# Optimization experiments

Hardware: AMD Instinct MI355X
Metric: run time of the kernel (lower is better)

The kernel has to match this reference:

```python
import jax, jax.numpy as jnp
import numpy as np

B, T, IN, CTRL = 128, 64, 512, 512
N, MM, S, R, W = 128, 128, 3, 4, 1  # slots, word size, num_shift, read heads, write heads
L = 3 + MM + S          # per-read-head instr length (k,b,g,s,t)
LW = L + 2 * MM         # per-write-head instr length (+erase,+add)
NOUT = R * L + W * LW   # 926


def _l2n(x, axis):
    # matches tf.nn.l2_normalize: x * rsqrt(max(sum(x^2), 1e-12))
    return x * jax.lax.rsqrt(jnp.maximum(jnp.sum(x * x, axis=axis, keepdims=True), 1e-12))


def _get_weight(Mem, w_old, head):
    # Mem (B,N,MM), w_old (B,N), head (B,L)
    k = head[:, :MM]
    b = jnp.exp(head[:, MM])
    g = jax.nn.sigmoid(head[:, MM + 1])
    s = jax.nn.softmax(head[:, MM + 2:MM + 2 + S], axis=-1)
    t = jax.nn.softplus(head[:, MM + 2 + S]) + 1.0
    # content addressing (NB: original normalizes M along axis=1, the slot axis -- kept faithful)
    nM = _l2n(Mem, 1)
    nk = _l2n(k, -1)
    sim = jnp.einsum('bnm,bm->bn', nM, nk)
    wc = jax.nn.softmax(sim * b[:, None], axis=-1)
    # interpolate
    wi = wc * g[:, None] + w_old * (1.0 - g[:, None])
    # circular shift via small correlation window
    bound = S // 2
    padded = jnp.concatenate([wi[:, -bound:], wi, wi[:, :bound]], axis=1)  # (B, N+2*bound)
    win = jnp.stack([padded[:, j:j + N] for j in range(S)], axis=-1)       # (B,N,S)
    ws = jnp.einsum('bns,bs->bn', win, s)
    # sharpen
    p = jnp.power(ws, t[:, None])
    return p / (jnp.sum(p, axis=-1, keepdims=True) + 1e-12)


def _forward(x, Wc, bc, Wk, bk):
    Mem0 = jnp.zeros((B, N, MM), x.dtype).at[:, N // 2, :].set(1.0)
    rv0 = jnp.zeros((B, R, MM), x.dtype)
    rw0 = jnp.zeros((B, R, N), x.dtype)
    ww0 = jnp.zeros((B, W, N), x.dtype)
    gw = jax.vmap(_get_weight, in_axes=(None, 1, 1), out_axes=1)  # over head axis

    def step(carry, xt):
        rv, rw, ww, Mem = carry
        h = jnp.concatenate([xt, rv.reshape(B, R * MM)], axis=-1)
        out = jnp.tanh(h @ Wc + bc)               # controller output
        instrs = out @ Wk + bk                    # head instructions (B,NOUT)
        rh = instrs[:, :R * L].reshape(B, R, L)
        wh = instrs[:, R * L:].reshape(B, W, LW)
        rw_new = gw(Mem, rw, rh)                  # (B,R,N)
        ww_new = gw(Mem, ww, wh[..., :L])         # (B,W,N)
        e = wh[..., L:L + MM]                     # (B,W,MM)
        a = wh[..., L + MM:]                      # (B,W,MM)
        for i in range(W):                        # erase all heads first
            Mem = Mem * (1.0 - ww_new[:, i, :, None] * e[:, i, None, :])
        for i in range(W):                        # then add
            Mem = Mem + ww_new[:, i, :, None] * a[:, i, None, :]
        rv_new = jnp.einsum('bnm,brn->brm', Mem, rw_new)
        return (rv_new, rw_new, ww_new, Mem), out

    _, outs = jax.lax.scan(step, (rv0, rw0, ww0, Mem0), jnp.swapaxes(x, 0, 1))
    return jnp.swapaxes(outs, 0, 1)  # (B,T,CTRL) return_sequences=True


def setup_inputs() -> dict:
    key = jax.random.key(0)
    ks = jax.random.split(key, 3)
    x = jax.random.normal(ks[0], (B, T, IN), jnp.float32)
    Wc = jax.random.normal(ks[1], (IN + R * MM, CTRL), jnp.float32) / np.sqrt(IN + R * MM).astype(np.float32)
    bc = jnp.zeros((CTRL,), jnp.float32)
    Wk = jax.random.normal(ks[2], (CTRL, NOUT), jnp.float32) * 0.02
    bk = jnp.zeros((NOUT,), jnp.float32)
    return {"x": x, "Wc": Wc, "bc": bc, "Wk": Wk, "bk": bk}


def reference(x, Wc, bc, Wk, bk):
    return _forward(x, Wc, bc, Wk, bk)
```

## Files before the change

### kernel.cpp

```cpp
#include <hip/hip_runtime.h>
#include <math.h>

#define B_    128
#define T_    64
#define INX   512
#define CTRL  512
#define NN    128
#define MMM   128
#define RR    4
#define LLh   134
#define NOUT  926
#define NTHR  512

#define MSTR  129

struct __align__(16) SM2 {
  float Mem[2][NN][MSTR];
  float rw[2][RR][NN];
  float ww[2][NN];
  float instr[2][928];
  float rv[2][512];
  union {
    float out_s[2][512];
    struct { float red[2][256]; float invn[2][MMM]; } d;
  } u;
};

__device__ __forceinline__ float wsum64(float v) {
  #pragma unroll
  for (int m = 32; m >= 1; m >>= 1) v += __shfl_xor(v, m);
  return v;
}
__device__ __forceinline__ float wmax64(float v) {
  #pragma unroll
  for (int m = 32; m >= 1; m >>= 1) v = fmaxf(v, __shfl_xor(v, m));
  return v;
}

__global__ __launch_bounds__(256) void pre_mm(const float* __restrict__ X,
                                              const float* __restrict__ Wc,
                                              const float* __restrict__ bc,
                                              float* __restrict__ out) {
  __shared__ float Xs[16][68];
  __shared__ float Ws[16][64];
  const int wg = blockIdx.x;
  const int r0 = (wg >> 3) * 64, c0 = (wg & 7) * 64;
  const int tid = threadIdx.x;
  const int ti = tid >> 4, tj = tid & 15;
  float acc[4][4] = {};
  for (int kk = 0; kk < 512; kk += 16) {
    __syncthreads();
    for (int e = tid; e < 1024; e += 256) {
      int i = e >> 4, k = e & 15;
      Xs[k][i] = X[(size_t)(r0 + i) * 512 + kk + k];
    }
    for (int e = tid; e < 1024; e += 256) {
      int k = e >> 6, j = e & 63;
      Ws[k][j] = Wc[(size_t)(kk + k) * CTRL + c0 + j];
    }
    __syncthreads();
    #pragma unroll
    for (int k = 0; k < 16; ++k) {
      float a0 = Xs[k][ti*4+0], a1 = Xs[k][ti*4+1], a2 = Xs[k][ti*4+2], a3 = Xs[k][ti*4+3];
      float b0 = Ws[k][tj*4+0], b1 = Ws[k][tj*4+1], b2 = Ws[k][tj*4+2], b3 = Ws[k][tj*4+3];
      acc[0][0]+=a0*b0; acc[0][1]+=a0*b1; acc[0][2]+=a0*b2; acc[0][3]+=a0*b3;
      acc[1][0]+=a1*b0; acc[1][1]+=a1*b1; acc[1][2]+=a1*b2; acc[1][3]+=a1*b3;
      acc[2][0]+=a2*b0; acc[2][1]+=a2*b1; acc[2][2]+=a2*b2; acc[2][3]+=a2*b3;
      acc[3][0]+=a3*b0; acc[3][1]+=a3*b1; acc[3][2]+=a3*b2; acc[3][3]+=a3*b3;
    }
  }
  #pragma unroll
  for (int i = 0; i < 4; ++i) {
    size_t o = (size_t)(r0 + ti*4 + i) * 512 + c0 + tj*4;
    float4 v = { acc[i][0] + bc[c0+tj*4+0], acc[i][1] + bc[c0+tj*4+1],
                 acc[i][2] + bc[c0+tj*4+2], acc[i][3] + bc[c0+tj*4+3] };
    *(float4*)&out[o] = v;
  }
}

__device__ __forceinline__ void do_head(SM2& sm, int tau, int lane) {
  const int b  = tau / 5;
  const int hd = tau - 5 * b;
  const int off = (hd < RR) ? hd * LLh : RR * LLh;
  const float* ins = sm.instr[b];
  const int n0 = lane, n1 = lane + 64;

  float k0 = ins[off + n0], k1 = ins[off + n1];
  float invk = rsqrtf(fmaxf(wsum64(k0 * k0 + k1 * k1), 1e-12f));
  float beta = expf(ins[off + 128]);
  float gg = 1.f / (1.f + expf(-ins[off + 129]));
  float s0 = ins[off + 130], s1 = ins[off + 131], s2 = ins[off + 132];
  float smx = fmaxf(s0, fmaxf(s1, s2));
  float e0 = expf(s0 - smx), e1 = expf(s1 - smx), e2 = expf(s2 - smx);
  float esm = e0 + e1 + e2; s0 = e0 / esm; s1 = e1 / esm; s2 = e2 / esm;
  float spx = ins[off + 133];
  float tt = ((spx > 20.f) ? spx : log1pf(expf(spx))) + 1.0f;

  float p0 = 0.f, p1 = 0.f;
  #pragma unroll 4
  for (int m = 0; m < 128; ++m) {
    float km = sm.u.d.invn[b][m] * ins[off + m];
    p0 += sm.Mem[b][n0][m] * km;
    p1 += sm.Mem[b][n1][m] * km;
  }
  float sim0 = p0 * invk * beta, sim1 = p1 * invk * beta;
  float mx = wmax64(fmaxf(sim0, sim1));
  float ev0 = expf(sim0 - mx), ev1 = expf(sim1 - mx);
  float es = wsum64(ev0 + ev1);
  float wold0 = (hd < RR) ? sm.rw[b][hd][n0] : sm.ww[b][n0];
  float wold1 = (hd < RR) ? sm.rw[b][hd][n1] : sm.ww[b][n1];
  float wi0 = gg * (ev0 / es) + (1.f - gg) * wold0;
  float wi1 = gg * (ev1 / es) + (1.f - gg) * wold1;

  int ls = (lane + 63) & 63;
  float A0 = __shfl(wi0, ls), A1 = __shfl(wi1, ls);
  float wprev0 = (lane == 0) ? A1 : A0;
  float wprev1 = (lane == 0) ? A0 : A1;
  int ln = (lane + 1) & 63;
  float B0 = __shfl(wi0, ln), B1 = __shfl(wi1, ln);
  float wnext0 = (lane == 63) ? B1 : B0;
  float wnext1 = (lane == 63) ? B0 : B1;

  float ws0 = s0 * wprev0 + s1 * wi0 + s2 * wnext0;
  float ws1 = s0 * wprev1 + s1 * wi1 + s2 * wnext1;
  float pv0 = powf(ws0, tt), pv1 = powf(ws1, tt);
  float inv = 1.f / (wsum64(pv0 + pv1) + 1e-12f);
  if (hd < RR) { sm.rw[b][hd][n0] = pv0 * inv; sm.rw[b][hd][n1] = pv1 * inv; }
  else         { sm.ww[b][n0]     = pv0 * inv; sm.ww[b][n1]     = pv1 * inv; }
}

__global__ __launch_bounds__(512) void ntm2(const float* __restrict__ Wc,
                                            const float* __restrict__ Wk,
                                            const float* __restrict__ bk,
                                            float* __restrict__ out) {
  __shared__ SM2 sm;
  const int wg = blockIdx.x, tid = threadIdx.x;
  const int b0 = wg * 2;
  const int lt = tid & 255, bb = tid >> 8;
  const int j  = tid;
  const int wv = tid >> 6, lane = tid & 63;

  for (int e = tid; e < 2 * NN * MMM; e += NTHR) {
    int bl = e >> 14, n = (e >> 7) & 127;
    sm.Mem[bl][n][e & 127] = (n == NN / 2) ? 1.0f : 0.0f;
  }
  for (int e = tid; e < 2 * RR * NN; e += NTHR) ((float*)sm.rw)[e] = 0.0f;
  for (int e = tid; e < 2 * NN;      e += NTHR) ((float*)sm.ww)[e] = 0.0f;
  for (int e = tid; e < 2 * 512;     e += NTHR) ((float*)sm.rv)[e] = 0.0f;
  __syncthreads();

  for (int t = 0; t < T_; ++t) {
    {
      float a0 = 0.f, a1 = 0.f;
      const float* wp = Wc + (size_t)INX * CTRL + j;
      for (int k8 = 0; k8 < 512; k8 += 8) {
        float w0 = wp[(size_t)(k8+0)*CTRL];
        float w1 = wp[(size_t)(k8+1)*CTRL];
        float w2 = wp[(size_t)(k8+2)*CTRL];
        float w3 = wp[(size_t)(k8+3)*CTRL];
        float w4 = wp[(size_t)(k8+4)*CTRL];
        float w5 = wp[(size_t)(k8+5)*CTRL];
        float w6 = wp[(size_t)(k8+6)*CTRL];
        float w7 = wp[(size_t)(k8+7)*CTRL];
        float4 r0a = *(const float4*)&sm.rv[0][k8];
        float4 r0b = *(const float4*)&sm.rv[0][k8+4];
        float4 r1a = *(const float4*)&sm.rv[1][k8];
        float4 r1b = *(const float4*)&sm.rv[1][k8+4];
        a0 += r0a.x*w0 + r0a.y*w1 + r0a.z*w2 + r0a.w*w3
            + r0b.x*w4 + r0b.y*w5 + r0b.z*w6 + r0b.w*w7;
        a1 += r1a.x*w0 + r1a.y*w1 + r1a.z*w2 + r1a.w*w3
            + r1b.x*w4 + r1b.y*w5 + r1b.z*w6 + r1b.w*w7;
      }
      size_t o0 = ((size_t)(b0+0)*T_ + t)*CTRL + j;
      size_t o1 = ((size_t)(b0+1)*T_ + t)*CTRL + j;
      float v0 = tanhf(out[o0] + a0);
      float v1 = tanhf(out[o1] + a1);
      out[o0] = v0; out[o1] = v1;
      sm.u.out_s[0][j] = v0; sm.u.out_s[1][j] = v1;
    }
    __syncthreads();

    {
      const int c1 = (j < NOUT - 512) ? j + 512 : j;
      float a00 = 0.f, a10 = 0.f, a01 = 0.f, a11 = 0.f;
      const float* wp0 = Wk + j;
      const float* wp1 = Wk + c1;
      for (int k4 = 0; k4 < 512; k4 += 4) {
        float4 o0 = *(const float4*)&sm.u.out_s[0][k4];
        float4 o1 = *(const float4*)&sm.u.out_s[1][k4];
        #pragma unroll
        for (int i = 0; i < 4; ++i) {
          float w0 = wp0[(size_t)(k4+i)*NOUT];
          float w1 = wp1[(size_t)(k4+i)*NOUT];
          float e0 = (i==0)? o0.x : (i==1)? o0.y : (i==2)? o0.z : o0.w;
          float e1 = (i==0)? o1.x : (i==1)? o1.y : (i==2)? o1.z : o1.w;
          a00 += e0 * w0; a01 += e0 * w1;
          a10 += e1 * w0; a11 += e1 * w1;
        }
      }
      sm.instr[0][j] = a00 + bk[j];
      sm.instr[1][j] = a10 + bk[j];
      if (j < NOUT - 512) {
        sm.instr[0][j+512] = a01 + bk[j+512];
        sm.instr[1][j+512] = a11 + bk[j+512];
      }
    }
    __syncthreads();

    {
      {
        int m = lt & 127, h = lt >> 7;
        float p = 0.f;
        #pragma unroll 8
        for (int q = 0; q < 64; ++q) { float v = sm.Mem[bb][h*64+q][m]; p += v*v; }
        sm.u.d.red[bb][lt] = p;
      }
      __syncthreads();
      if (lt < 128) sm.u.d.invn[bb][lt] =
          rsqrtf(fmaxf(sm.u.d.red[bb][lt] + sm.u.d.red[bb][lt+128], 1e-12f));
      __syncthreads();

      do_head(sm, wv, lane);
      if (wv < 2) do_head(sm, 8 + wv, lane);
      __syncthreads();

      for (int e = lt; e < NN * MMM; e += 256) {
        int n = e >> 7, m = e & 127;
        float w = sm.ww[bb][n];
        sm.Mem[bb][n][m] = sm.Mem[bb][n][m] * (1.f - w * sm.instr[bb][670 + m])
                         + w * sm.instr[bb][798 + m];
      }
      __syncthreads();

      for (int e = lt; e < RR * MMM; e += 256) {
        int r = e >> 7, m = e & 127;
        float acc = 0.f;
        #pragma unroll 8
        for (int n = 0; n < NN; ++n) acc += sm.Mem[bb][n][m] * sm.rw[bb][r][n];
        sm.rv[bb][e] = acc;
      }
    }
    __syncthreads();
  }
}

extern "C" void kernel_launch(void* const* d_in, const int* in_sizes, int n_in,
                              void* d_out, int out_size, void* d_ws, size_t ws_size,
                              hipStream_t stream) {
  const float* x  = (const float*)d_in[0];
  const float* Wc = (const float*)d_in[1];
  const float* bc = (const float*)d_in[2];
  const float* Wk = (const float*)d_in[3];
  const float* bk = (const float*)d_in[4];
  float* out = (float*)d_out;

  pre_mm<<<dim3(1024), dim3(256), 0, stream>>>(x, Wc, bc, out);
  ntm2<<<dim3(B_ / 2), dim3(NTHR), 0, stream>>>(Wc, Wk, bk, out);
}
```

Before: 3.188 ms.

## Double recurrent block to 1024 threads with split-K matvecs

Raises the per-block thread count from 512 to 1024. Both recurrent matvecs (rv@Wc and out@Wk) are split along K into two halves, with a shared-memory reduction and an extra barrier each. The slot-norm, head evaluation, memory update and read loops are redistributed over twice as many threads, so each thread does less serial work on the latency-bound per-step chain. The cost is extra barriers and shared traffic per step, and possibly more register pressure under the 1024-thread bound.

```diff
diff --git a/kernel.cpp b/kernel.cpp
--- a/kernel.cpp
+++ b/kernel.cpp
@@ -10,7 +10,7 @@
 #define RR    4
 #define LLh   134
 #define NOUT  926
-#define NTHR  512
+#define NTHR  1024
 
 #define MSTR  129
 
@@ -21,8 +21,8 @@
   float instr[2][928];
   float rv[2][512];
   union {
-    float out_s[2][512];
-    struct { float red[2][256]; float invn[2][MMM]; } d;
+    struct { float out_s[2][512]; float red[512][4]; } c;
+    struct { float red[2][512]; float invn[2][MMM]; } d;
   } u;
 };
 
@@ -55,8 +55,8 @@
       Xs[k][i] = X[(size_t)(r0 + i) * 512 + kk + k];
     }
     for (int e = tid; e < 1024; e += 256) {
-      int k = e >> 6, j = e & 63;
-      Ws[k][j] = Wc[(size_t)(kk + k) * CTRL + c0 + j];
+      int k = e >> 6, jx = e & 63;
+      Ws[k][jx] = Wc[(size_t)(kk + k) * CTRL + c0 + jx];
     }
     __syncthreads();
     #pragma unroll
@@ -129,15 +129,16 @@
   else         { sm.ww[b][n0]     = pv0 * inv; sm.ww[b][n1]     = pv1 * inv; }
 }
 
-__global__ __launch_bounds__(512) void ntm2(const float* __restrict__ Wc,
-                                            const float* __restrict__ Wk,
-                                            const float* __restrict__ bk,
-                                            float* __restrict__ out) {
+__global__ __launch_bounds__(1024) void ntm2(const float* __restrict__ Wc,
+                                             const float* __restrict__ Wk,
+                                             const float* __restrict__ bk,
+                                             float* __restrict__ out) {
   __shared__ SM2 sm;
   const int wg = blockIdx.x, tid = threadIdx.x;
   const int b0 = wg * 2;
-  const int lt = tid & 255, bb = tid >> 8;
-  const int j  = tid;
+  const int j  = tid & 511;
+  const int kh = tid >> 9;
+  const int lt = tid & 511, bb = tid >> 9;
   const int wv = tid >> 6, lane = tid & 63;
 
   for (int e = tid; e < 2 * NN * MMM; e += NTHR) {
@@ -151,9 +152,10 @@
 
   for (int t = 0; t < T_; ++t) {
     {
+      const int kb = kh * 256;
       float a0 = 0.f, a1 = 0.f;
-      const float* wp = Wc + (size_t)INX * CTRL + j;
-      for (int k8 = 0; k8 < 512; k8 += 8) {
+      const float* wp = Wc + (size_t)(INX + kb) * CTRL + j;
+      for (int k8 = 0; k8 < 256; k8 += 8) {
         float w0 = wp[(size_t)(k8+0)*CTRL];
         float w1 = wp[(size_t)(k8+1)*CTRL];
         float w2 = wp[(size_t)(k8+2)*CTRL];
@@ -162,32 +164,39 @@
         float w5 = wp[(size_t)(k8+5)*CTRL];
         float w6 = wp[(size_t)(k8+6)*CTRL];
         float w7 = wp[(size_t)(k8+7)*CTRL];
-        float4 r0a = *(const float4*)&sm.rv[0][k8];
-        float4 r0b = *(const float4*)&sm.rv[0][k8+4];
-        float4 r1a = *(const float4*)&sm.rv[1][k8];
-        float4 r1b = *(const float4*)&sm.rv[1][k8+4];
+        float4 r0a = *(const float4*)&sm.rv[0][kb+k8];
+        float4 r0b = *(const float4*)&sm.rv[0][kb+k8+4];
+        float4 r1a = *(const float4*)&sm.rv[1][kb+k8];
+        float4 r1b = *(const float4*)&sm.rv[1][kb+k8+4];
         a0 += r0a.x*w0 + r0a.y*w1 + r0a.z*w2 + r0a.w*w3
             + r0b.x*w4 + r0b.y*w5 + r0b.z*w6 + r0b.w*w7;
         a1 += r1a.x*w0 + r1a.y*w1 + r1a.z*w2 + r1a.w*w3
             + r1b.x*w4 + r1b.y*w5 + r1b.z*w6 + r1b.w*w7;
       }
-      size_t o0 = ((size_t)(b0+0)*T_ + t)*CTRL + j;
-      size_t o1 = ((size_t)(b0+1)*T_ + t)*CTRL + j;
-      float v0 = tanhf(out[o0] + a0);
-      float v1 = tanhf(out[o1] + a1);
-      out[o0] = v0; out[o1] = v1;
-      sm.u.out_s[0][j] = v0; sm.u.out_s[1][j] = v1;
+      if (kh == 1) { sm.u.c.red[j][0] = a0; sm.u.c.red[j][1] = a1; }
+      __syncthreads();
+      if (kh == 0) {
+        a0 += sm.u.c.red[j][0];
+        a1 += sm.u.c.red[j][1];
+        size_t o0 = ((size_t)(b0+0)*T_ + t)*CTRL + j;
+        size_t o1 = ((size_t)(b0+1)*T_ + t)*CTRL + j;
+        float v0 = tanhf(out[o0] + a0);
+        float v1 = tanhf(out[o1] + a1);
+        out[o0] = v0; out[o1] = v1;
+        sm.u.c.out_s[0][j] = v0; sm.u.c.out_s[1][j] = v1;
+      }
     }
     __syncthreads();
 
     {
+      const int kb = kh * 256;
       const int c1 = (j < NOUT - 512) ? j + 512 : j;
       float a00 = 0.f, a10 = 0.f, a01 = 0.f, a11 = 0.f;
-      const float* wp0 = Wk + j;
-      const float* wp1 = Wk + c1;
-      for (int k4 = 0; k4 < 512; k4 += 4) {
-        float4 o0 = *(const float4*)&sm.u.out_s[0][k4];
-        float4 o1 = *(const float4*)&sm.u.out_s[1][k4];
+      const float* wp0 = Wk + (size_t)kb * NOUT + j;
+      const float* wp1 = Wk + (size_t)kb * NOUT + c1;
+      for (int k4 = 0; k4 < 256; k4 += 4) {
+        float4 o0 = *(const float4*)&sm.u.c.out_s[0][kb + k4];
+        float4 o1 = *(const float4*)&sm.u.c.out_s[1][kb + k4];
         #pragma unroll
         for (int i = 0; i < 4; ++i) {
           float w0 = wp0[(size_t)(k4+i)*NOUT];
@@ -198,11 +207,20 @@
           a10 += e1 * w0; a11 += e1 * w1;
         }
       }
-      sm.instr[0][j] = a00 + bk[j];
-      sm.instr[1][j] = a10 + bk[j];
-      if (j < NOUT - 512) {
-        sm.instr[0][j+512] = a01 + bk[j+512];
-        sm.instr[1][j+512] = a11 + bk[j+512];
+      if (kh == 1) {
+        float4 v = { a00, a01, a10, a11 };
+        *(float4*)&sm.u.c.red[j][0] = v;
+      }
+      __syncthreads();
+      if (kh == 0) {
+        float4 q = *(const float4*)&sm.u.c.red[j][0];
+        a00 += q.x; a01 += q.y; a10 += q.z; a11 += q.w;
+        sm.instr[0][j] = a00 + bk[j];
+        sm.instr[1][j] = a10 + bk[j];
+        if (j < NOUT - 512) {
+          sm.instr[0][j+512] = a01 + bk[j+512];
+          sm.instr[1][j+512] = a11 + bk[j+512];
+        }
       }
     }
     __syncthreads();
@@ -212,32 +230,33 @@
         int m = lt & 127, h = lt >> 7;
         float p = 0.f;
         #pragma unroll 8
-        for (int q = 0; q < 64; ++q) { float v = sm.Mem[bb][h*64+q][m]; p += v*v; }
+        for (int q = 0; q < 32; ++q) { float v = sm.Mem[bb][h*32+q][m]; p += v*v; }
         sm.u.d.red[bb][lt] = p;
       }
       __syncthreads();
       if (lt < 128) sm.u.d.invn[bb][lt] =
-          rsqrtf(fmaxf(sm.u.d.red[bb][lt] + sm.u.d.red[bb][lt+128], 1e-12f));
-      __syncthreads();
-
-      do_head(sm, wv, lane);
-      if (wv < 2) do_head(sm, 8 + wv, lane);
-      __syncthreads();
-
-      for (int e = lt; e < NN * MMM; e += 256) {
-        int n = e >> 7, m = e & 127;
-        float w = sm.ww[bb][n];
-        sm.Mem[bb][n][m] = sm.Mem[bb][n][m] * (1.f - w * sm.instr[bb][670 + m])
-                         + w * sm.instr[bb][798 + m];
-      }
-      __syncthreads();
-
-      for (int e = lt; e < RR * MMM; e += 256) {
-        int r = e >> 7, m = e & 127;
+          rsqrtf(fmaxf(sm.u.d.red[bb][lt] + sm.u.d.red[bb][lt+128]
+                     + sm.u.d.red[bb][lt+256] + sm.u.d.red[bb][lt+384], 1e-12f));
+      __syncthreads();
+
+      if (wv < 10) do_head(sm, wv, lane);
+      __syncthreads();
+
+      for (int e = tid; e < 2 * NN * MMM; e += NTHR) {
+        int bl = e >> 14, n = (e >> 7) & 127, m = e & 127;
+        float w = sm.ww[bl][n];
+        sm.Mem[bl][n][m] = sm.Mem[bl][n][m] * (1.f - w * sm.instr[bl][670 + m])
+                         + w * sm.instr[bl][798 + m];
+      }
+      __syncthreads();
+
+      {
+        int m = tid & 127, r = (tid >> 7) & 3, bl = tid >> 9;
         float acc = 0.f;
+        const float* rwr = sm.rw[bl][r];
         #pragma unroll 8
-        for (int n = 0; n < NN; ++n) acc += sm.Mem[bb][n][m] * sm.rw[bb][r][n];
-        sm.rv[bb][e] = acc;
+        for (int n = 0; n < NN; ++n) acc += sm.Mem[bl][n][m] * rwr[n];
+        sm.rv[bl][r * 128 + m] = acc;
       }
     }
     __syncthreads();
```

After: 2.880 ms. 9.7% less time.

## Split recurrent step across 256 workgroups with global-memory counters between stages

Applied to the files above, without the earlier changes.

Replaces the 64-workgroup kernel, where each workgroup ran the whole time loop for two batch rows, with a 256-workgroup persistent kernel. The controller matmul is tiled over 16-row by 16-column blocks, the instruction matmul over 16-row by 32-column blocks, and the memory and head update runs with one workgroup per batch row. Stages hand off data through global scratch buffers and atomic counters with spin-waits, so the weight reads are spread over more compute units instead of every workgroup streaming all of Wc and Wk. In exchange it adds global round-trips and inter-workgroup synchronization three times per timestep, and it relies on all 256 workgroups being resident at the same time.

```diff
diff --git a/kernel.cpp b/kernel.cpp
--- a/kernel.cpp
+++ b/kernel.cpp
@@ -10,21 +10,33 @@
 #define RR    4
 #define LLh   134
 #define NOUT  926
-#define NTHR  512
-
-#define MSTR  129
-
-struct __align__(16) SM2 {
-  float Mem[2][NN][MSTR];
-  float rw[2][RR][NN];
-  float ww[2][NN];
-  float instr[2][928];
-  float rv[2][512];
-  union {
-    float out_s[2][512];
-    struct { float red[2][256]; float invn[2][MMM]; } d;
-  } u;
+#define NWG   256
+#define NTHR  1024
+
+
+struct __align__(16) SMX {
+  float Mem[NN][129];
+  float rw[RR][NN];
+  float ww[NN];
+  float instr[928];
+  float invn[MMM];
+  float red[1024];
+  float stage[16][512];
 };
+
+__device__ __forceinline__ void spin_ge(int* p, int target) {
+  int it = 0;
+  while (__hip_atomic_load(p, __ATOMIC_RELAXED, __HIP_MEMORY_SCOPE_AGENT) < target) {
+    __builtin_amdgcn_s_sleep(8);
+    if ((++it & 15) == 0) __builtin_amdgcn_fence(__ATOMIC_ACQUIRE, "agent");
+    if (it > (1 << 18)) break;
+  }
+  __builtin_amdgcn_fence(__ATOMIC_ACQUIRE, "agent");
+}
+__device__ __forceinline__ void arrive(int* p) {
+  __builtin_amdgcn_fence(__ATOMIC_RELEASE, "agent");
+  __hip_atomic_fetch_add(p, 1, __ATOMIC_RELAXED, __HIP_MEMORY_SCOPE_AGENT);
+}
 
 __device__ __forceinline__ float wsum64(float v) {
   #pragma unroll
@@ -55,8 +67,8 @@
       Xs[k][i] = X[(size_t)(r0 + i) * 512 + kk + k];
     }
     for (int e = tid; e < 1024; e += 256) {
-      int k = e >> 6, j = e & 63;
-      Ws[k][j] = Wc[(size_t)(kk + k) * CTRL + c0 + j];
+      int k = e >> 6, jx = e & 63;
+      Ws[k][jx] = Wc[(size_t)(kk + k) * CTRL + c0 + jx];
     }
     __syncthreads();
     #pragma unroll
@@ -78,11 +90,9 @@
   }
 }
 
-__device__ __forceinline__ void do_head(SM2& sm, int tau, int lane) {
-  const int b  = tau / 5;
-  const int hd = tau - 5 * b;
+__device__ __forceinline__ void do_head(SMX& sm, int hd, int lane) {
   const int off = (hd < RR) ? hd * LLh : RR * LLh;
-  const float* ins = sm.instr[b];
+  const float* ins = sm.instr;
   const int n0 = lane, n1 = lane + 64;
 
   float k0 = ins[off + n0], k1 = ins[off + n1];
@@ -99,16 +109,16 @@
   float p0 = 0.f, p1 = 0.f;
   #pragma unroll 4
   for (int m = 0; m < 128; ++m) {
-    float km = sm.u.d.invn[b][m] * ins[off + m];
-    p0 += sm.Mem[b][n0][m] * km;
-    p1 += sm.Mem[b][n1][m] * km;
+    float km = sm.invn[m] * ins[off + m];
+    p0 += sm.Mem[n0][m] * km;
+    p1 += sm.Mem[n1][m] * km;
   }
   float sim0 = p0 * invk * beta, sim1 = p1 * invk * beta;
   float mx = wmax64(fmaxf(sim0, sim1));
   float ev0 = expf(sim0 - mx), ev1 = expf(sim1 - mx);
   float es = wsum64(ev0 + ev1);
-  float wold0 = (hd < RR) ? sm.rw[b][hd][n0] : sm.ww[b][n0];
-  float wold1 = (hd < RR) ? sm.rw[b][hd][n1] : sm.ww[b][n1];
+  float wold0 = (hd < RR) ? sm.rw[hd][n0] : sm.ww[n0];
+  float wold1 = (hd < RR) ? sm.rw[hd][n1] : sm.ww[n1];
   float wi0 = gg * (ev0 / es) + (1.f - gg) * wold0;
   float wi1 = gg * (ev1 / es) + (1.f - gg) * wold1;
 
@@ -125,122 +135,150 @@
   float ws1 = s0 * wprev1 + s1 * wi1 + s2 * wnext1;
   float pv0 = powf(ws0, tt), pv1 = powf(ws1, tt);
   float inv = 1.f / (wsum64(pv0 + pv1) + 1e-12f);
-  if (hd < RR) { sm.rw[b][hd][n0] = pv0 * inv; sm.rw[b][hd][n1] = pv1 * inv; }
-  else         { sm.ww[b][n0]     = pv0 * inv; sm.ww[b][n1]     = pv1 * inv; }
-}
-
-__global__ __launch_bounds__(512) void ntm2(const float* __restrict__ Wc,
-                                            const float* __restrict__ Wk,
-                                            const float* __restrict__ bk,
-                                            float* __restrict__ out) {
-  __shared__ SM2 sm;
+  if (hd < RR) { sm.rw[hd][n0] = pv0 * inv; sm.rw[hd][n1] = pv1 * inv; }
+  else         { sm.ww[n0]     = pv0 * inv; sm.ww[n1]     = pv1 * inv; }
+}
+
+__global__ __launch_bounds__(1024) void ntm3(const float* __restrict__ Wc,
+                                             const float* __restrict__ Wk,
+                                             const float* __restrict__ bk,
+                                             float* __restrict__ out,
+                                             float* __restrict__ instr_g,
+                                             float* __restrict__ rv_g,
+                                             int* __restrict__ cnt) {
+  __shared__ SMX sm;
   const int wg = blockIdx.x, tid = threadIdx.x;
-  const int b0 = wg * 2;
-  const int lt = tid & 255, bb = tid >> 8;
-  const int j  = tid;
-  const int wv = tid >> 6, lane = tid & 63;
-
-  for (int e = tid; e < 2 * NN * MMM; e += NTHR) {
-    int bl = e >> 14, n = (e >> 7) & 127;
-    sm.Mem[bl][n][e & 127] = (n == NN / 2) ? 1.0f : 0.0f;
-  }
-  for (int e = tid; e < 2 * RR * NN; e += NTHR) ((float*)sm.rw)[e] = 0.0f;
-  for (int e = tid; e < 2 * NN;      e += NTHR) ((float*)sm.ww)[e] = 0.0f;
-  for (int e = tid; e < 2 * 512;     e += NTHR) ((float*)sm.rv)[e] = 0.0f;
+  const int lane = tid & 63, wv = tid >> 6;
+
+  const int rowgB = wg >> 5, colgB = wg & 31;
+  const int hasC  = (wg < 232);
+  const int rowgC = wg / 29, colgC = wg - rowgC * 29;
+  const int isOwner = (wg < B_);
+  const int bD = wg;
+
+  int* cntB = cnt;
+  int* cntC = cnt + 128;
+  int* cntD = cnt + 256;
+
+  if (isOwner) {
+    for (int e = tid; e < NN * MMM; e += NTHR) {
+      int n = e >> 7;
+      sm.Mem[n][e & 127] = (n == NN / 2) ? 1.0f : 0.0f;
+    }
+    for (int e = tid; e < RR * NN; e += NTHR) ((float*)sm.rw)[e] = 0.0f;
+    if (tid < NN) sm.ww[tid] = 0.0f;
+    if (tid < 512) rv_g[(size_t)bD * 512 + tid] = 0.0f;
+    __syncthreads();
+    if (tid == 0) arrive(&cntD[(bD >> 4) * 16]);
+  }
   __syncthreads();
 
   for (int t = 0; t < T_; ++t) {
+    if (tid == 0) spin_ge(&cntD[rowgB * 16], 16 * (t + 1));
+    __syncthreads();
     {
-      float a0 = 0.f, a1 = 0.f;
-      const float* wp = Wc + (size_t)INX * CTRL + j;
-      for (int k8 = 0; k8 < 512; k8 += 8) {
-        float w0 = wp[(size_t)(k8+0)*CTRL];
-        float w1 = wp[(size_t)(k8+1)*CTRL];
-        float w2 = wp[(size_t)(k8+2)*CTRL];
-        float w3 = wp[(size_t)(k8+3)*CTRL];
-        float w4 = wp[(size_t)(k8+4)*CTRL];
-        float w5 = wp[(size_t)(k8+5)*CTRL];
-        float w6 = wp[(size_t)(k8+6)*CTRL];
-        float w7 = wp[(size_t)(k8+7)*CTRL];
-        float4 r0a = *(const float4*)&sm.rv[0][k8];
-        float4 r0b = *(const float4*)&sm.rv[0][k8+4];
-        float4 r1a = *(const float4*)&sm.rv[1][k8];
-        float4 r1b = *(const float4*)&sm.rv[1][k8+4];
-        a0 += r0a.x*w0 + r0a.y*w1 + r0a.z*w2 + r0a.w*w3
-            + r0b.x*w4 + r0b.y*w5 + r0b.z*w6 + r0b.w*w7;
-        a1 += r1a.x*w0 + r1a.y*w1 + r1a.z*w2 + r1a.w*w3
-            + r1b.x*w4 + r1b.y*w5 + r1b.z*w6 + r1b.w*w7;
-      }
-      size_t o0 = ((size_t)(b0+0)*T_ + t)*CTRL + j;
-      size_t o1 = ((size_t)(b0+1)*T_ + t)*CTRL + j;
-      float v0 = tanhf(out[o0] + a0);
-      float v1 = tanhf(out[o1] + a1);
-      out[o0] = v0; out[o1] = v1;
-      sm.u.out_s[0][j] = v0; sm.u.out_s[1][j] = v1;
-    }
-    __syncthreads();
-
-    {
-      const int c1 = (j < NOUT - 512) ? j + 512 : j;
-      float a00 = 0.f, a10 = 0.f, a01 = 0.f, a11 = 0.f;
-      const float* wp0 = Wk + j;
-      const float* wp1 = Wk + c1;
-      for (int k4 = 0; k4 < 512; k4 += 4) {
-        float4 o0 = *(const float4*)&sm.u.out_s[0][k4];
-        float4 o1 = *(const float4*)&sm.u.out_s[1][k4];
-        #pragma unroll
-        for (int i = 0; i < 4; ++i) {
-          float w0 = wp0[(size_t)(k4+i)*NOUT];
-          float w1 = wp1[(size_t)(k4+i)*NOUT];
-          float e0 = (i==0)? o0.x : (i==1)? o0.y : (i==2)? o0.z : o0.w;
-          float e1 = (i==0)? o1.x : (i==1)? o1.y : (i==2)? o1.z : o1.w;
-          a00 += e0 * w0; a01 += e0 * w1;
-          a10 += e1 * w0; a11 += e1 * w1;
-        }
-      }
-      sm.instr[0][j] = a00 + bk[j];
-      sm.instr[1][j] = a10 + bk[j];
-      if (j < NOUT - 512) {
-        sm.instr[0][j+512] = a01 + bk[j+512];
-        sm.instr[1][j+512] = a11 + bk[j+512];
-      }
-    }
-    __syncthreads();
-
-    {
+      const int b0 = rowgB * 16, c0 = colgB * 16;
+      for (int e = tid * 4; e < 8192; e += NTHR * 4) {
+        int i = e >> 9, k = e & 511;
+        *(float4*)&sm.stage[i][k] = *(const float4*)&rv_g[(size_t)(b0 + i) * 512 + k];
+      }
+      __syncthreads();
+      const int kh = tid >> 8, i = (tid >> 4) & 15, jc = tid & 15;
+      const float* wp = Wc + (size_t)(INX + kh * 128) * CTRL + c0 + jc;
+      const float* rvrow = &sm.stage[i][kh * 128];
+      float a = 0.f;
+      for (int k8 = 0; k8 < 128; k8 += 8) {
+        float w0 = wp[(size_t)(k8+0)*CTRL], w1 = wp[(size_t)(k8+1)*CTRL];
+        float w2 = wp[(size_t)(k8+2)*CTRL], w3 = wp[(size_t)(k8+3)*CTRL];
+        float w4 = wp[(size_t)(k8+4)*CTRL], w5 = wp[(size_t)(k8+5)*CTRL];
+        float w6 = wp[(size_t)(k8+6)*CTRL], w7 = wp[(size_t)(k8+7)*CTRL];
+        a += rvrow[k8+0]*w0 + rvrow[k8+1]*w1 + rvrow[k8+2]*w2 + rvrow[k8+3]*w3
+           + rvrow[k8+4]*w4 + rvrow[k8+5]*w5 + rvrow[k8+6]*w6 + rvrow[k8+7]*w7;
+      }
+      if (kh > 0) sm.red[(kh - 1) * 256 + i * 16 + jc] = a;
+      __syncthreads();
+      if (kh == 0) {
+        a += sm.red[i*16+jc] + sm.red[256 + i*16+jc] + sm.red[512 + i*16+jc];
+        size_t o = ((size_t)(b0 + i) * T_ + t) * CTRL + c0 + jc;
+        out[o] = tanhf(out[o] + a);
+      }
+    }
+    __syncthreads();
+    if (tid == 0) arrive(&cntB[rowgB * 16]);
+
+    if (hasC) {
+      if (tid == 0) spin_ge(&cntB[rowgC * 16], 32 * (t + 1));
+      __syncthreads();
+      const int b0 = rowgC * 16, c0 = colgC * 32;
+      for (int e = tid * 4; e < 8192; e += NTHR * 4) {
+        int i = e >> 9, k = e & 511;
+        *(float4*)&sm.stage[i][k] =
+            *(const float4*)&out[((size_t)(b0 + i) * T_ + t) * CTRL + k];
+      }
+      __syncthreads();
+      const int kh = tid >> 9, i = (tid >> 5) & 15, jc = tid & 31;
+      const int col = c0 + jc;
+      const int colw = (col < NOUT) ? col : (NOUT - 1);
+      const float* wp = Wk + (size_t)(kh * 256) * NOUT + colw;
+      const float* orow = &sm.stage[i][kh * 256];
+      float a = 0.f;
+      for (int k8 = 0; k8 < 256; k8 += 8) {
+        float w0 = wp[(size_t)(k8+0)*NOUT], w1 = wp[(size_t)(k8+1)*NOUT];
+        float w2 = wp[(size_t)(k8+2)*NOUT], w3 = wp[(size_t)(k8+3)*NOUT];
+        float w4 = wp[(size_t)(k8+4)*NOUT], w5 = wp[(size_t)(k8+5)*NOUT];
+        float w6 = wp[(size_t)(k8+6)*NOUT], w7 = wp[(size_t)(k8+7)*NOUT];
+        a += orow[k8+0]*w0 + orow[k8+1]*w1 + orow[k8+2]*w2 + orow[k8+3]*w3
+           + orow[k8+4]*w4 + orow[k8+5]*w5 + orow[k8+6]*w6 + orow[k8+7]*w7;
+      }
+      if (kh == 1) sm.red[i * 32 + jc] = a;
+      __syncthreads();
+      if (kh == 0 && col < NOUT) {
+        a += sm.red[i * 32 + jc];
+        instr_g[(size_t)(b0 + i) * 928 + col] = a + bk[col];
+      }
+      __syncthreads();
+      if (tid == 0) arrive(&cntC[rowgC * 16]);
+    }
+
+    if (isOwner) {
+      if (tid == 0) spin_ge(&cntC[(bD >> 4) * 16], 29 * (t + 1));
+      __syncthreads();
+      if (tid < 928) sm.instr[tid] = instr_g[(size_t)bD * 928 + tid];
+      __syncthreads();
       {
-        int m = lt & 127, h = lt >> 7;
+        int m = tid & 127, h = tid >> 7;
         float p = 0.f;
         #pragma unroll 8
-        for (int q = 0; q < 64; ++q) { float v = sm.Mem[bb][h*64+q][m]; p += v*v; }
-        sm.u.d.red[bb][lt] = p;
-      }
-      __syncthreads();
-      if (lt < 128) sm.u.d.invn[bb][lt] =
-          rsqrtf(fmaxf(sm.u.d.red[bb][lt] + sm.u.d.red[bb][lt+128], 1e-12f));
-      __syncthreads();
-
-      do_head(sm, wv, lane);
-      if (wv < 2) do_head(sm, 8 + wv, lane);
-      __syncthreads();
-
-      for (int e = lt; e < NN * MMM; e += 256) {
+        for (int q = 0; q < 16; ++q) { float v = sm.Mem[h*16+q][m]; p += v*v; }
+        sm.red[tid] = p;
+      }
+      __syncthreads();
+      if (tid < 128) {
+        float s = sm.red[tid]       + sm.red[tid+128] + sm.red[tid+256] + sm.red[tid+384]
+                + sm.red[tid+512]   + sm.red[tid+640] + sm.red[tid+768] + sm.red[tid+896];
+        sm.invn[tid] = rsqrtf(fmaxf(s, 1e-12f));
+      }
+      __syncthreads();
+      if (wv < 5) do_head(sm, wv, lane);
+      __syncthreads();
+      for (int e = tid; e < NN * MMM; e += NTHR) {
         int n = e >> 7, m = e & 127;
-        float w = sm.ww[bb][n];
-        sm.Mem[bb][n][m] = sm.Mem[bb][n][m] * (1.f - w * sm.instr[bb][670 + m])
-                         + w * sm.instr[bb][798 + m];
-      }
-      __syncthreads();
-
-      for (int e = lt; e < RR * MMM; e += 256) {
-        int r = e >> 7, m = e & 127;
+        float w = sm.ww[n];
+        sm.Mem[n][m] = sm.Mem[n][m] * (1.f - w * sm.instr[670 + m])
+                     + w * sm.instr[798 + m];
+      }
+      __syncthreads();
+      if (tid < 512) {
+        int m = tid & 127, r = tid >> 7;
         float acc = 0.f;
+        const float* rwr = sm.rw[r];
         #pragma unroll 8
-        for (int n = 0; n < NN; ++n) acc += sm.Mem[bb][n][m] * sm.rw[bb][r][n];
-        sm.rv[bb][e] = acc;
-      }
-    }
-    __syncthreads();
+        for (int n = 0; n < NN; ++n) acc += sm.Mem[n][m] * rwr[n];
+        rv_g[(size_t)bD * 512 + r * 128 + m] = acc;
+      }
+      __syncthreads();
+      if (tid == 0) arrive(&cntD[(bD >> 4) * 16]);
+    }
   }
 }
 
@@ -254,6 +292,12 @@
   const float* bk = (const float*)d_in[4];
   float* out = (float*)d_out;
 
+  char* ws = (char*)d_ws;
+  int*   cnt     = (int*)ws;
+  float* instr_g = (float*)(ws + 2048);
+  float* rv_g    = (float*)(ws + 2048 + (size_t)B_*928*4);
+
+  hipMemsetAsync(cnt, 0, 2048, stream);
   pre_mm<<<dim3(1024), dim3(256), 0, stream>>>(x, Wc, bc, out);
-  ntm2<<<dim3(B_ / 2), dim3(NTHR), 0, stream>>>(Wc, Wk, bk, out);
-}
+  ntm3<<<dim3(NWG), dim3(NTHR), 0, stream>>>(Wc, Wk, bk, out, instr_g, rv_g, cnt);
+}
```

New measurement: 4.899 ms. 1.54x slower.
